# Kernel tuning notes

Hardware: AMD Instinct MI355X
Metric: run time of the kernel (lower is better)

Reference implementation:

```python
import jax, jax.numpy as jnp
import numpy as np

B, S, D, H, L, V = 2, 2048, 256, 4, 4, 50257
HD = D // H  # head_dim = 64


def layer_norm(x, scale, bias, eps=1e-5):
    m = jnp.mean(x, axis=-1, keepdims=True)
    v = jnp.var(x, axis=-1, keepdims=True)
    return (x - m) * jax.lax.rsqrt(v + eps) * scale + bias


def setup_inputs() -> dict:
    key = jax.random.key(0)
    ks = jax.random.split(key, 16)

    def w(k, shape, std=0.02):
        return (jax.random.normal(k, shape) * std).astype(jnp.float32)

    return {
        "input_ids": jax.random.randint(ks[0], (B, S), 0, V, dtype=jnp.int32),
        "tok_emb": w(ks[1], (V, D)),      # tied with lm_head
        "pos_emb": w(ks[2], (S, D)),
        # per-layer params stacked on leading L axis (scanned)
        "Wq": w(ks[3], (L, D, D)), "bq": jnp.zeros((L, D), jnp.float32),
        "Wk": w(ks[4], (L, D, D)), "bk": jnp.zeros((L, D), jnp.float32),
        "Wv": w(ks[5], (L, D, D)), "bv": jnp.zeros((L, D), jnp.float32),
        "Wo": w(ks[6], (L, D, D)), "bo": jnp.zeros((L, D), jnp.float32),
        "ln1_s": jnp.ones((L, D), jnp.float32), "ln1_b": jnp.zeros((L, D), jnp.float32),
        "ln2_s": jnp.ones((L, D), jnp.float32), "ln2_b": jnp.zeros((L, D), jnp.float32),
        "W1": w(ks[7], (L, D, 4 * D)), "b1": jnp.zeros((L, 4 * D), jnp.float32),
        "W2": w(ks[8], (L, 4 * D, D)), "b2": jnp.zeros((L, D), jnp.float32),
        "lnf_s": jnp.ones((D,), jnp.float32), "lnf_b": jnp.zeros((D,), jnp.float32),
    }


def _forward(input_ids, tok_emb, pos_emb, Wq, bq, Wk, bk, Wv, bv, Wo, bo,
             ln1_s, ln1_b, ln2_s, ln2_b, W1, b1, W2, b2, lnf_s, lnf_b):
    Bv, Sv = input_ids.shape
    h = tok_emb[input_ids] + pos_emb[:Sv][None, :, :]  # (B,S,D); dropout = eval no-op
    scale = HD ** -0.5
    causal = jnp.tril(jnp.ones((Sv, Sv), dtype=bool))  # (S,S)

    def block(h, p):
        wq, bq_, wk, bk_, wv, bv_, wo, bo_, s1, sb1, s2, sb2, wf1, bf1, wf2, bf2 = p
        n = layer_norm(h, s1, sb1)
        q = (n @ wq + bq_).reshape(Bv, Sv, H, HD)
        k = (n @ wk + bk_).reshape(Bv, Sv, H, HD)
        v = (n @ wv + bv_).reshape(Bv, Sv, H, HD)
        scores = jnp.einsum('bqhd,bkhd->bhqk', q, k) * scale  # (B,H,S,S)
        scores = jnp.where(causal, scores, -jnp.inf)
        attn = jax.nn.softmax(scores, axis=-1)  # attn dropout = eval no-op
        o = jnp.einsum('bhqk,bkhd->bqhd', attn, v).reshape(Bv, Sv, D)
        h = h + (o @ wo + bo_)
        n2 = layer_norm(h, s2, sb2)
        f = jax.nn.gelu(n2 @ wf1 + bf1, approximate=False) @ wf2 + bf2  # torch GELU = exact erf
        return h + f, None

    params = (Wq, bq, Wk, bk, Wv, bv, Wo, bo, ln1_s, ln1_b, ln2_s, ln2_b, W1, b1, W2, b2)
    h, _ = jax.lax.scan(block, h, params)
    h = layer_norm(h, lnf_s, lnf_b)
    return h @ tok_emb.T  # tied lm_head, (B,S,V)


def reference(input_ids, tok_emb, pos_emb, Wq, bq, Wk, bk, Wv, bv, Wo, bo,
              ln1_s, ln1_b, ln2_s, ln2_b, W1, b1, W2, b2, lnf_s, lnf_b):
    return _forward(input_ids, tok_emb, pos_emb, Wq, bq, Wk, bk, Wv, bv, Wo, bo,
                    ln1_s, ln1_b, ln2_s, ln2_b, W1, b1, W2, b2, lnf_s, lnf_b)
```

## Files before the change

kernel.cpp:

```cpp
#include <hip/hip_runtime.h>

#define BB   2
#define SS   2048
#define DD   256
#define HH   4
#define LL   4
#define VV   50257
#define HDIM 64
#define DFF  1024
#define BS   (BB*SS)

typedef unsigned short u16;
typedef unsigned int   u32;
typedef __attribute__((ext_vector_type(8))) short bf16x8;
typedef __attribute__((ext_vector_type(4))) float f32x4;

#define DEV static __device__ __forceinline__

DEV u16 f2bf(float f) {
    u32 x = __builtin_bit_cast(u32, f);
    x += 0x7fffu + ((x >> 16) & 1u);
    return (u16)(x >> 16);
}

DEV f32x4 zero4() { f32x4 v; v[0]=0.f; v[1]=0.f; v[2]=0.f; v[3]=0.f; return v; }

__global__ __launch_bounds__(256) void cvt_kernel(const float* __restrict__ in,
                                                  u16* __restrict__ out, int n4) {
    int i = blockIdx.x * 256 + threadIdx.x;
    if (i >= n4) return;
    float4 v = ((const float4*)in)[i];
    ushort4 o; o.x = f2bf(v.x); o.y = f2bf(v.y); o.z = f2bf(v.z); o.w = f2bf(v.w);
    ((ushort4*)out)[i] = o;
}

__global__ __launch_bounds__(256) void wtrans_kernel(const float* __restrict__ in,
                                                     u16* __restrict__ out, int K, int N) {
    __shared__ float tile[32][33];
    const size_t off = (size_t)blockIdx.z * K * N;
    in  += off; out += off;
    int tx = threadIdx.x, ty = threadIdx.y;
    int n0 = blockIdx.x * 32, k0 = blockIdx.y * 32;
    #pragma unroll
    for (int i = 0; i < 4; i++)
        tile[ty + 8*i][tx] = in[(size_t)(k0 + ty + 8*i) * N + n0 + tx];
    __syncthreads();
    #pragma unroll
    for (int i = 0; i < 4; i++)
        out[(size_t)(n0 + ty + 8*i) * K + k0 + tx] = f2bf(tile[tx][ty + 8*i]);
}

__global__ __launch_bounds__(256) void embed_kernel(const int* __restrict__ ids,
                                                    const float* __restrict__ te,
                                                    const float* __restrict__ pe,
                                                    float* __restrict__ h) {
    int i  = blockIdx.x * 256 + threadIdx.x;
    int bs = i >> 6, c = i & 63;
    int id = ids[bs];
    int sr = bs & (SS - 1);
    float4 t = ((const float4*)(te + (size_t)id * DD))[c];
    float4 p = ((const float4*)(pe + (size_t)sr * DD))[c];
    float4 r; r.x = t.x + p.x; r.y = t.y + p.y; r.z = t.z + p.z; r.w = t.w + p.w;
    ((float4*)h)[i] = r;
}

__global__ __launch_bounds__(256) void ln_kernel(const float* __restrict__ x,
                                                 const float* __restrict__ g,
                                                 const float* __restrict__ b,
                                                 u16* __restrict__ out) {
    const int wid = threadIdx.x >> 6, lane = threadIdx.x & 63;
    const int row = blockIdx.x * 4 + wid;
    const float4 v = ((const float4*)(x + (size_t)row * DD))[lane];
    float s = v.x + v.y + v.z + v.w;
    float q = v.x*v.x + v.y*v.y + v.z*v.z + v.w*v.w;
    #pragma unroll
    for (int m = 1; m < 64; m <<= 1) { s += __shfl_xor(s, m); q += __shfl_xor(q, m); }
    const float mean = s * (1.f / DD);
    const float var  = q * (1.f / DD) - mean * mean;
    const float rs   = rsqrtf(var + 1e-5f);
    const float4 gg = ((const float4*)g)[lane];
    const float4 bb = ((const float4*)b)[lane];
    ushort4 o;
    o.x = f2bf((v.x - mean) * rs * gg.x + bb.x);
    o.y = f2bf((v.y - mean) * rs * gg.y + bb.y);
    o.z = f2bf((v.z - mean) * rs * gg.z + bb.z);
    o.w = f2bf((v.w - mean) * rs * gg.w + bb.w);
    ((ushort4*)(out + (size_t)row * DD))[lane] = o;
}

template<int BM, int BN, int EPI>
__global__ __launch_bounds__(256) void gemm_kernel(const u16* __restrict__ A,
                                                   const u16* __restrict__ Bt,
                                                   const float* __restrict__ bias,
                                                   const float* res, void* outp,
                                                   int M, int N, int K) {
    constexpr int NI = BM / 32, NJ = BN / 32;
    __shared__ __align__(16) u16 As[BM * 72];
    __shared__ __align__(16) u16 Bs[BN * 72];
    const int tid = threadIdx.x;
    const int wid = tid >> 6, lane = tid & 63, quad = lane >> 4, l16 = lane & 15;
    const int m0 = blockIdx.y * BM, n0 = blockIdx.x * BN;
    const int wm = (wid >> 1) * (BM / 2), wn = (wid & 1) * (BN / 2);

    f32x4 acc[NI][NJ];
    #pragma unroll
    for (int i = 0; i < NI; i++)
        #pragma unroll
        for (int j = 0; j < NJ; j++) acc[i][j] = zero4();

    for (int k0 = 0; k0 < K; k0 += 64) {
        #pragma unroll
        for (int p = 0; p < BM / 32; p++) {
            int idx = p * 256 + tid, row = idx >> 3, c = (idx & 7) * 8;
            *(uint4*)(&As[row * 72 + c]) =
                *(const uint4*)(A + (size_t)(m0 + row) * K + k0 + c);
        }
        #pragma unroll
        for (int p = 0; p < BN / 32; p++) {
            int idx = p * 256 + tid, row = idx >> 3, c = (idx & 7) * 8;
            uint4 val{0, 0, 0, 0};
            if (EPI != 3 || (n0 + row) < N)
                val = *(const uint4*)(Bt + (size_t)(n0 + row) * K + k0 + c);
            *(uint4*)(&Bs[row * 72 + c]) = val;
        }
        __syncthreads();
        #pragma unroll
        for (int ks = 0; ks < 2; ks++) {
            bf16x8 af[NI], bfr[NJ];
            #pragma unroll
            for (int i = 0; i < NI; i++)
                af[i] = *(const bf16x8*)(&As[(wm + i*16 + l16) * 72 + ks*32 + quad*8]);
            #pragma unroll
            for (int j = 0; j < NJ; j++)
                bfr[j] = *(const bf16x8*)(&Bs[(wn + j*16 + l16) * 72 + ks*32 + quad*8]);
            #pragma unroll
            for (int i = 0; i < NI; i++)
                #pragma unroll
                for (int j = 0; j < NJ; j++)
                    acc[i][j] = __builtin_amdgcn_mfma_f32_16x16x32_bf16(
                        af[i], bfr[j], acc[i][j], 0, 0, 0);
        }
        __syncthreads();
    }

    #pragma unroll
    for (int i = 0; i < NI; i++) {
        #pragma unroll
        for (int j = 0; j < NJ; j++) {
            #pragma unroll
            for (int r = 0; r < 4; r++) {
                int row = m0 + wm + i*16 + quad*4 + r;
                int col = n0 + wn + j*16 + l16;
                float v = acc[i][j][r];
                if (EPI == 0) {
                    v += bias[col];
                    ((u16*)outp)[(size_t)row * N + col] = f2bf(v);
                } else if (EPI == 1) {
                    v += bias[col];
                    float gel = 0.5f * v * (1.f + erff(v * 0.70710678118654752f));
                    ((u16*)outp)[(size_t)row * N + col] = f2bf(gel);
                } else if (EPI == 2) {
                    v += bias[col] + res[(size_t)row * N + col];
                    ((float*)outp)[(size_t)row * N + col] = v;
                } else {
                    if (col < N) ((float*)outp)[(size_t)row * N + col] = v;
                }
            }
        }
    }
}

__global__ __launch_bounds__(256) void vtrans_kernel(const u16* __restrict__ v,
                                                     u16* __restrict__ vt) {
    __shared__ u16 tile[32][33];
    int bh = blockIdx.z, b = bh >> 2, hh = bh & 3;
    int s0 = blockIdx.x * 32, d0 = blockIdx.y * 32;
    int tx = threadIdx.x, ty = threadIdx.y;
    #pragma unroll
    for (int i = 0; i < 4; i++)
        tile[ty + 8*i][tx] = v[(size_t)(b*SS + s0 + ty + 8*i) * DD + hh*HDIM + d0 + tx];
    __syncthreads();
    #pragma unroll
    for (int i = 0; i < 4; i++)
        vt[(size_t)(bh*HDIM + d0 + ty + 8*i) * SS + s0 + tx] = tile[tx][ty + 8*i];
}

__global__ __launch_bounds__(256) void attn_kernel(const u16* __restrict__ q,
                                                   const u16* __restrict__ k,
                                                   const u16* __restrict__ vt,
                                                   u16* __restrict__ o) {
    const int tid = threadIdx.x;
    const int wid = tid >> 6, lane = tid & 63, quad = lane >> 4, l16 = lane & 15;
    const int bh = blockIdx.y, b = bh >> 2, hh = bh & 3;
    const int wgq0 = blockIdx.x * 64;
    const int wq0  = wgq0 + wid * 16;

    __shared__ __align__(16) u16 plds[4][16 * 40];

    const u16* qb = q  + (size_t)b * SS * DD + hh * HDIM;
    const u16* kb = k  + (size_t)b * SS * DD + hh * HDIM;
    const u16* vb = vt + (size_t)bh * HDIM * SS;

    bf16x8 qf0 = *(const bf16x8*)(qb + (size_t)(wq0 + l16) * DD + quad * 8);
    bf16x8 qf1 = *(const bf16x8*)(qb + (size_t)(wq0 + l16) * DD + 32 + quad * 8);

    f32x4 oacc[4];
    #pragma unroll
    for (int i = 0; i < 4; i++) oacc[i] = zero4();
    float mst[4], lst[4];
    #pragma unroll
    for (int r = 0; r < 4; r++) { mst[r] = -1e30f; lst[r] = 0.f; }

    const int nt = wgq0 / 32 + 2;
    for (int kt = 0; kt < nt; ++kt) {
        const int kv0 = kt * 32;
        f32x4 sc[2]; sc[0] = zero4(); sc[1] = zero4();
        #pragma unroll
        for (int t = 0; t < 2; t++) {
            const u16* kr = kb + (size_t)(kv0 + t*16 + l16) * DD + quad * 8;
            bf16x8 kf0 = *(const bf16x8*)(kr);
            bf16x8 kf1 = *(const bf16x8*)(kr + 32);
            sc[t] = __builtin_amdgcn_mfma_f32_16x16x32_bf16(qf0, kf0, sc[t], 0, 0, 0);
            sc[t] = __builtin_amdgcn_mfma_f32_16x16x32_bf16(qf1, kf1, sc[t], 0, 0, 0);
        }
        float mx[4];
        #pragma unroll
        for (int r = 0; r < 4; r++) {
            int qrow = wq0 + quad * 4 + r;
            float s0 = sc[0][r] * 0.125f; if (kv0 + l16 > qrow)      s0 = -1e30f;
            float s1 = sc[1][r] * 0.125f; if (kv0 + 16 + l16 > qrow) s1 = -1e30f;
            sc[0][r] = s0; sc[1][r] = s1;
            mx[r] = fmaxf(s0, s1);
        }
        #pragma unroll
        for (int m = 1; m < 16; m <<= 1) {
            #pragma unroll
            for (int r = 0; r < 4; r++) mx[r] = fmaxf(mx[r], __shfl_xor(mx[r], m));
        }
        float al[4], rsum[4];
        #pragma unroll
        for (int r = 0; r < 4; r++) {
            float mn = fmaxf(mst[r], mx[r]);
            al[r] = __expf(mst[r] - mn);
            mst[r] = mn;
            float p0 = __expf(sc[0][r] - mn);
            float p1 = __expf(sc[1][r] - mn);
            sc[0][r] = p0; sc[1][r] = p1;
            rsum[r] = p0 + p1;
        }
        #pragma unroll
        for (int m = 1; m < 16; m <<= 1) {
            #pragma unroll
            for (int r = 0; r < 4; r++) rsum[r] += __shfl_xor(rsum[r], m);
        }
        #pragma unroll
        for (int r = 0; r < 4; r++) lst[r] = lst[r] * al[r] + rsum[r];
        #pragma unroll
        for (int d4 = 0; d4 < 4; d4++)
            #pragma unroll
            for (int r = 0; r < 4; r++) oacc[d4][r] *= al[r];

        u16* pw = &plds[wid][0];
        #pragma unroll
        for (int r = 0; r < 4; r++) {
            pw[(quad*4 + r) * 40 + l16]      = f2bf(sc[0][r]);
            pw[(quad*4 + r) * 40 + 16 + l16] = f2bf(sc[1][r]);
        }
        __syncthreads();
        bf16x8 pf = *(const bf16x8*)(pw + l16 * 40 + quad * 8);
        #pragma unroll
        for (int d4 = 0; d4 < 4; d4++) {
            bf16x8 vf = *(const bf16x8*)(vb + (size_t)(d4*16 + l16) * SS + kv0 + quad * 8);
            oacc[d4] = __builtin_amdgcn_mfma_f32_16x16x32_bf16(pf, vf, oacc[d4], 0, 0, 0);
        }
        __syncthreads();
    }

    u16* ob = o + (size_t)b * SS * DD + hh * HDIM;
    #pragma unroll
    for (int d4 = 0; d4 < 4; d4++)
        #pragma unroll
        for (int r = 0; r < 4; r++) {
            float ov = oacc[d4][r] / lst[r];
            ob[(size_t)(wq0 + quad*4 + r) * DD + d4*16 + l16] = f2bf(ov);
        }
}

extern "C" void kernel_launch(void* const* d_in, const int* in_sizes, int n_in,
                              void* d_out, int out_size, void* d_ws, size_t ws_size,
                              hipStream_t stream) {
    (void)in_sizes; (void)n_in; (void)out_size; (void)ws_size;
    const int*   ids  = (const int*)  d_in[0];
    const float* temb = (const float*)d_in[1];
    const float* pemb = (const float*)d_in[2];
    const float* Wq = (const float*)d_in[3];  const float* bq = (const float*)d_in[4];
    const float* Wk = (const float*)d_in[5];  const float* bk = (const float*)d_in[6];
    const float* Wv = (const float*)d_in[7];  const float* bv = (const float*)d_in[8];
    const float* Wo = (const float*)d_in[9];  const float* bo = (const float*)d_in[10];
    const float* ln1s = (const float*)d_in[11]; const float* ln1b = (const float*)d_in[12];
    const float* ln2s = (const float*)d_in[13]; const float* ln2b = (const float*)d_in[14];
    const float* W1 = (const float*)d_in[15]; const float* b1 = (const float*)d_in[16];
    const float* W2 = (const float*)d_in[17]; const float* b2 = (const float*)d_in[18];
    const float* lnfs = (const float*)d_in[19]; const float* lnfb = (const float*)d_in[20];
    float* out = (float*)d_out;

    char* ws = (char*)d_ws;
    auto alloc = [&](size_t bytes) -> char* {
        char* p = ws; ws += (bytes + 255) & ~(size_t)255; return p;
    };
    u16* tembb = (u16*)alloc((size_t)VV * DD * 2);
    u16* wqt   = (u16*)alloc((size_t)LL * DD * DD * 2);
    u16* wkt   = (u16*)alloc((size_t)LL * DD * DD * 2);
    u16* wvt   = (u16*)alloc((size_t)LL * DD * DD * 2);
    u16* wot   = (u16*)alloc((size_t)LL * DD * DD * 2);
    u16* w1t   = (u16*)alloc((size_t)LL * DD * DFF * 2);
    u16* w2t   = (u16*)alloc((size_t)LL * DD * DFF * 2);
    float* h   = (float*)alloc((size_t)BS * DD * 4);
    u16* nbuf  = (u16*)alloc((size_t)BS * DD * 2);
    u16* qbuf  = (u16*)alloc((size_t)BS * DD * 2);
    u16* kbuf  = (u16*)alloc((size_t)BS * DD * 2);
    u16* vbuf  = (u16*)alloc((size_t)BS * DD * 2);
    u16* vtb   = (u16*)alloc((size_t)BS * DD * 2);
    u16* obuf  = (u16*)alloc((size_t)BS * DD * 2);
    u16* f1    = (u16*)alloc((size_t)BS * DFF * 2);

    cvt_kernel<<<(VV*DD/4 + 255)/256, 256, 0, stream>>>(temb, tembb, VV*DD/4);
    wtrans_kernel<<<dim3(DD/32, DD/32, LL),  dim3(32,8), 0, stream>>>(Wq, wqt, DD, DD);
    wtrans_kernel<<<dim3(DD/32, DD/32, LL),  dim3(32,8), 0, stream>>>(Wk, wkt, DD, DD);
    wtrans_kernel<<<dim3(DD/32, DD/32, LL),  dim3(32,8), 0, stream>>>(Wv, wvt, DD, DD);
    wtrans_kernel<<<dim3(DD/32, DD/32, LL),  dim3(32,8), 0, stream>>>(Wo, wot, DD, DD);
    wtrans_kernel<<<dim3(DFF/32, DD/32, LL), dim3(32,8), 0, stream>>>(W1, w1t, DD, DFF);
    wtrans_kernel<<<dim3(DD/32, DFF/32, LL), dim3(32,8), 0, stream>>>(W2, w2t, DFF, DD);

    embed_kernel<<<BS*DD/4/256, 256, 0, stream>>>(ids, temb, pemb, h);

    const dim3 gQ(DD/64, BS/64);
    for (int l = 0; l < LL; l++) {
        ln_kernel<<<BS/4, 256, 0, stream>>>(h, ln1s + l*DD, ln1b + l*DD, nbuf);
        gemm_kernel<64,64,0><<<gQ, 256, 0, stream>>>(nbuf, wqt + (size_t)l*DD*DD,
            bq + l*DD, nullptr, qbuf, BS, DD, DD);
        gemm_kernel<64,64,0><<<gQ, 256, 0, stream>>>(nbuf, wkt + (size_t)l*DD*DD,
            bk + l*DD, nullptr, kbuf, BS, DD, DD);
        gemm_kernel<64,64,0><<<gQ, 256, 0, stream>>>(nbuf, wvt + (size_t)l*DD*DD,
            bv + l*DD, nullptr, vbuf, BS, DD, DD);
        vtrans_kernel<<<dim3(SS/32, HDIM/32, BB*HH), dim3(32,8), 0, stream>>>(vbuf, vtb);
        attn_kernel<<<dim3(SS/64, BB*HH), 256, 0, stream>>>(qbuf, kbuf, vtb, obuf);
        gemm_kernel<64,64,2><<<gQ, 256, 0, stream>>>(obuf, wot + (size_t)l*DD*DD,
            bo + l*DD, h, h, BS, DD, DD);
        ln_kernel<<<BS/4, 256, 0, stream>>>(h, ln2s + l*DD, ln2b + l*DD, nbuf);
        gemm_kernel<128,128,1><<<dim3(DFF/128, BS/128), 256, 0, stream>>>(nbuf,
            w1t + (size_t)l*DD*DFF, b1 + l*DFF, nullptr, f1, BS, DFF, DD);
        gemm_kernel<64,64,2><<<gQ, 256, 0, stream>>>(f1, w2t + (size_t)l*DD*DFF,
            b2 + l*DD, h, h, BS, DD, DFF);
    }
    ln_kernel<<<BS/4, 256, 0, stream>>>(h, lnfs, lnfb, nbuf);
    gemm_kernel<128,128,3><<<dim3((VV + 127)/128, BS/128), 256, 0, stream>>>(nbuf,
        tembb, nullptr, nullptr, out, BS, VV, DD);
}
```

Before: 1.859 ms.

## Fuse QKV projections into one GEMM and streamline attention inner loop

Concatenates Wq/Wk/Wv (and biases) into a single 768-wide weight so one GEMM produces Q, K and V into an interleaved buffer, removing two launches and re-reads of the normalized input. The attention kernel reads Q/K directly from this buffer with stride 768, prefetches the next K tile, loads V before the score MFMAs, and drops block-wide barriers since each wave uses its own LDS region. Each wave now iterates only over key tiles up to its own causal limit, skipping fully masked work. Relies on intra-wave LDS write/read ordering without a barrier.

```diff
diff --git a/kernel.cpp b/kernel.cpp
--- a/kernel.cpp
+++ b/kernel.cpp
@@ -9,6 +9,7 @@
 #define HDIM 64
 #define DFF  1024
 #define BS   (BB*SS)
+#define QKVS 768
 
 typedef unsigned short u16;
 typedef unsigned int   u32;
@@ -35,10 +36,11 @@
 }
 
 __global__ __launch_bounds__(256) void wtrans_kernel(const float* __restrict__ in,
-                                                     u16* __restrict__ out, int K, int N) {
+                                                     u16* __restrict__ out, int K, int N,
+                                                     size_t outLS) {
     __shared__ float tile[32][33];
-    const size_t off = (size_t)blockIdx.z * K * N;
-    in  += off; out += off;
+    in  += (size_t)blockIdx.z * K * N;
+    out += (size_t)blockIdx.z * outLS;
     int tx = threadIdx.x, ty = threadIdx.y;
     int n0 = blockIdx.x * 32, k0 = blockIdx.y * 32;
     #pragma unroll
@@ -48,6 +50,20 @@
     #pragma unroll
     for (int i = 0; i < 4; i++)
         out[(size_t)(n0 + ty + 8*i) * K + k0 + tx] = f2bf(tile[tx][ty + 8*i]);
+}
+
+__global__ __launch_bounds__(256) void bias_concat(const float* __restrict__ bq,
+                                                   const float* __restrict__ bk,
+                                                   const float* __restrict__ bv,
+                                                   float* __restrict__ out) {
+    int i = blockIdx.x * 256 + threadIdx.x;
+    if (i >= LL * QKVS) return;
+    int l = i / QKVS, c = i - l * QKVS;
+    float v;
+    if (c < DD)           v = bq[l * DD + c];
+    else if (c < 2 * DD)  v = bk[l * DD + c - DD];
+    else                  v = bv[l * DD + c - 2 * DD];
+    out[i] = v;
 }
 
 __global__ __launch_bounds__(256) void embed_kernel(const int* __restrict__ ids,
@@ -170,7 +186,7 @@
     }
 }
 
-__global__ __launch_bounds__(256) void vtrans_kernel(const u16* __restrict__ v,
+__global__ __launch_bounds__(256) void vtrans_kernel(const u16* __restrict__ qkv,
                                                      u16* __restrict__ vt) {
     __shared__ u16 tile[32][33];
     int bh = blockIdx.z, b = bh >> 2, hh = bh & 3;
@@ -178,58 +194,73 @@
     int tx = threadIdx.x, ty = threadIdx.y;
     #pragma unroll
     for (int i = 0; i < 4; i++)
-        tile[ty + 8*i][tx] = v[(size_t)(b*SS + s0 + ty + 8*i) * DD + hh*HDIM + d0 + tx];
+        tile[ty + 8*i][tx] =
+            qkv[(size_t)(b*SS + s0 + ty + 8*i) * QKVS + 2*DD + hh*HDIM + d0 + tx];
     __syncthreads();
     #pragma unroll
     for (int i = 0; i < 4; i++)
         vt[(size_t)(bh*HDIM + d0 + ty + 8*i) * SS + s0 + tx] = tile[tx][ty + 8*i];
 }
 
-__global__ __launch_bounds__(256) void attn_kernel(const u16* __restrict__ q,
-                                                   const u16* __restrict__ k,
+__global__ __launch_bounds__(256) void attn_kernel(const u16* __restrict__ qkv,
                                                    const u16* __restrict__ vt,
                                                    u16* __restrict__ o) {
     const int tid = threadIdx.x;
     const int wid = tid >> 6, lane = tid & 63, quad = lane >> 4, l16 = lane & 15;
     const int bh = blockIdx.y, b = bh >> 2, hh = bh & 3;
-    const int wgq0 = blockIdx.x * 64;
-    const int wq0  = wgq0 + wid * 16;
+    const int wq0 = blockIdx.x * 64 + wid * 16;
 
     __shared__ __align__(16) u16 plds[4][16 * 40];
 
-    const u16* qb = q  + (size_t)b * SS * DD + hh * HDIM;
-    const u16* kb = k  + (size_t)b * SS * DD + hh * HDIM;
+    const u16* qb = qkv + (size_t)b * SS * QKVS + hh * HDIM;
+    const u16* kb = qb + DD;
     const u16* vb = vt + (size_t)bh * HDIM * SS;
 
-    bf16x8 qf0 = *(const bf16x8*)(qb + (size_t)(wq0 + l16) * DD + quad * 8);
-    bf16x8 qf1 = *(const bf16x8*)(qb + (size_t)(wq0 + l16) * DD + 32 + quad * 8);
-
-    f32x4 oacc[4];
-    #pragma unroll
-    for (int i = 0; i < 4; i++) oacc[i] = zero4();
+    bf16x8 qf0 = *(const bf16x8*)(qb + (size_t)(wq0 + l16) * QKVS + quad * 8);
+    bf16x8 qf1 = *(const bf16x8*)(qb + (size_t)(wq0 + l16) * QKVS + 32 + quad * 8);
+
+    f32x4 oacc0 = zero4(), oacc1 = zero4(), oacc2 = zero4(), oacc3 = zero4();
     float mst[4], lst[4];
     #pragma unroll
     for (int r = 0; r < 4; r++) { mst[r] = -1e30f; lst[r] = 0.f; }
 
-    const int nt = wgq0 / 32 + 2;
+    const int nt = (wq0 >> 5) + 1;
+
+    const u16* krow = kb + (size_t)l16 * QKVS + quad * 8;
+    bf16x8 kc0 = *(const bf16x8*)(krow);
+    bf16x8 kc1 = *(const bf16x8*)(krow + 32);
+    bf16x8 kc2 = *(const bf16x8*)(krow + (size_t)16 * QKVS);
+    bf16x8 kc3 = *(const bf16x8*)(krow + (size_t)16 * QKVS + 32);
+
     for (int kt = 0; kt < nt; ++kt) {
         const int kv0 = kt * 32;
-        f32x4 sc[2]; sc[0] = zero4(); sc[1] = zero4();
-        #pragma unroll
-        for (int t = 0; t < 2; t++) {
-            const u16* kr = kb + (size_t)(kv0 + t*16 + l16) * DD + quad * 8;
-            bf16x8 kf0 = *(const bf16x8*)(kr);
-            bf16x8 kf1 = *(const bf16x8*)(kr + 32);
-            sc[t] = __builtin_amdgcn_mfma_f32_16x16x32_bf16(qf0, kf0, sc[t], 0, 0, 0);
-            sc[t] = __builtin_amdgcn_mfma_f32_16x16x32_bf16(qf1, kf1, sc[t], 0, 0, 0);
-        }
-        float mx[4];
+
+        bf16x8 vf0 = *(const bf16x8*)(vb + (size_t)(     l16) * SS + kv0 + quad * 8);
+        bf16x8 vf1 = *(const bf16x8*)(vb + (size_t)(16 + l16) * SS + kv0 + quad * 8);
+        bf16x8 vf2 = *(const bf16x8*)(vb + (size_t)(32 + l16) * SS + kv0 + quad * 8);
+        bf16x8 vf3 = *(const bf16x8*)(vb + (size_t)(48 + l16) * SS + kv0 + quad * 8);
+
+        f32x4 sc0 = zero4(), sc1 = zero4();
+        sc0 = __builtin_amdgcn_mfma_f32_16x16x32_bf16(qf0, kc0, sc0, 0, 0, 0);
+        sc0 = __builtin_amdgcn_mfma_f32_16x16x32_bf16(qf1, kc1, sc0, 0, 0, 0);
+        sc1 = __builtin_amdgcn_mfma_f32_16x16x32_bf16(qf0, kc2, sc1, 0, 0, 0);
+        sc1 = __builtin_amdgcn_mfma_f32_16x16x32_bf16(qf1, kc3, sc1, 0, 0, 0);
+
+        if (kt + 1 < nt) {
+            const u16* kr = kb + (size_t)(kv0 + 32 + l16) * QKVS + quad * 8;
+            kc0 = *(const bf16x8*)(kr);
+            kc1 = *(const bf16x8*)(kr + 32);
+            kc2 = *(const bf16x8*)(kr + (size_t)16 * QKVS);
+            kc3 = *(const bf16x8*)(kr + (size_t)16 * QKVS + 32);
+        }
+
+        float p0[4], p1[4], mx[4];
         #pragma unroll
         for (int r = 0; r < 4; r++) {
             int qrow = wq0 + quad * 4 + r;
-            float s0 = sc[0][r] * 0.125f; if (kv0 + l16 > qrow)      s0 = -1e30f;
-            float s1 = sc[1][r] * 0.125f; if (kv0 + 16 + l16 > qrow) s1 = -1e30f;
-            sc[0][r] = s0; sc[1][r] = s1;
+            float s0 = sc0[r] * 0.125f; if (kv0 + l16 > qrow)      s0 = -1e30f;
+            float s1 = sc1[r] * 0.125f; if (kv0 + 16 + l16 > qrow) s1 = -1e30f;
+            p0[r] = s0; p1[r] = s1;
             mx[r] = fmaxf(s0, s1);
         }
         #pragma unroll
@@ -243,10 +274,10 @@
             float mn = fmaxf(mst[r], mx[r]);
             al[r] = __expf(mst[r] - mn);
             mst[r] = mn;
-            float p0 = __expf(sc[0][r] - mn);
-            float p1 = __expf(sc[1][r] - mn);
-            sc[0][r] = p0; sc[1][r] = p1;
-            rsum[r] = p0 + p1;
+            float e0 = __expf(p0[r] - mn);
+            float e1 = __expf(p1[r] - mn);
+            p0[r] = e0; p1[r] = e1;
+            rsum[r] = e0 + e1;
         }
         #pragma unroll
         for (int m = 1; m < 16; m <<= 1) {
@@ -254,36 +285,35 @@
             for (int r = 0; r < 4; r++) rsum[r] += __shfl_xor(rsum[r], m);
         }
         #pragma unroll
-        for (int r = 0; r < 4; r++) lst[r] = lst[r] * al[r] + rsum[r];
-        #pragma unroll
-        for (int d4 = 0; d4 < 4; d4++)
-            #pragma unroll
-            for (int r = 0; r < 4; r++) oacc[d4][r] *= al[r];
+        for (int r = 0; r < 4; r++) {
+            lst[r] = lst[r] * al[r] + rsum[r];
+            oacc0[r] *= al[r]; oacc1[r] *= al[r];
+            oacc2[r] *= al[r]; oacc3[r] *= al[r];
+        }
 
         u16* pw = &plds[wid][0];
         #pragma unroll
         for (int r = 0; r < 4; r++) {
-            pw[(quad*4 + r) * 40 + l16]      = f2bf(sc[0][r]);
-            pw[(quad*4 + r) * 40 + 16 + l16] = f2bf(sc[1][r]);
-        }
-        __syncthreads();
+            pw[(quad*4 + r) * 40 + l16]      = f2bf(p0[r]);
+            pw[(quad*4 + r) * 40 + 16 + l16] = f2bf(p1[r]);
+        }
         bf16x8 pf = *(const bf16x8*)(pw + l16 * 40 + quad * 8);
-        #pragma unroll
-        for (int d4 = 0; d4 < 4; d4++) {
-            bf16x8 vf = *(const bf16x8*)(vb + (size_t)(d4*16 + l16) * SS + kv0 + quad * 8);
-            oacc[d4] = __builtin_amdgcn_mfma_f32_16x16x32_bf16(pf, vf, oacc[d4], 0, 0, 0);
-        }
-        __syncthreads();
+        oacc0 = __builtin_amdgcn_mfma_f32_16x16x32_bf16(pf, vf0, oacc0, 0, 0, 0);
+        oacc1 = __builtin_amdgcn_mfma_f32_16x16x32_bf16(pf, vf1, oacc1, 0, 0, 0);
+        oacc2 = __builtin_amdgcn_mfma_f32_16x16x32_bf16(pf, vf2, oacc2, 0, 0, 0);
+        oacc3 = __builtin_amdgcn_mfma_f32_16x16x32_bf16(pf, vf3, oacc3, 0, 0, 0);
     }
 
     u16* ob = o + (size_t)b * SS * DD + hh * HDIM;
     #pragma unroll
-    for (int d4 = 0; d4 < 4; d4++)
-        #pragma unroll
-        for (int r = 0; r < 4; r++) {
-            float ov = oacc[d4][r] / lst[r];
-            ob[(size_t)(wq0 + quad*4 + r) * DD + d4*16 + l16] = f2bf(ov);
-        }
+    for (int r = 0; r < 4; r++) {
+        const float inv = 1.f / lst[r];
+        const size_t row = (size_t)(wq0 + quad*4 + r) * DD;
+        ob[row +  0 + l16] = f2bf(oacc0[r] * inv);
+        ob[row + 16 + l16] = f2bf(oacc1[r] * inv);
+        ob[row + 32 + l16] = f2bf(oacc2[r] * inv);
+        ob[row + 48 + l16] = f2bf(oacc3[r] * inv);
+    }
 }
 
 extern "C" void kernel_launch(void* const* d_in, const int* in_sizes, int n_in,
@@ -309,42 +339,44 @@
         char* p = ws; ws += (bytes + 255) & ~(size_t)255; return p;
     };
     u16* tembb = (u16*)alloc((size_t)VV * DD * 2);
-    u16* wqt   = (u16*)alloc((size_t)LL * DD * DD * 2);
-    u16* wkt   = (u16*)alloc((size_t)LL * DD * DD * 2);
-    u16* wvt   = (u16*)alloc((size_t)LL * DD * DD * 2);
+    u16* wqkvt = (u16*)alloc((size_t)LL * QKVS * DD * 2);
     u16* wot   = (u16*)alloc((size_t)LL * DD * DD * 2);
     u16* w1t   = (u16*)alloc((size_t)LL * DD * DFF * 2);
     u16* w2t   = (u16*)alloc((size_t)LL * DD * DFF * 2);
+    float* bqkv= (float*)alloc((size_t)LL * QKVS * 4);
     float* h   = (float*)alloc((size_t)BS * DD * 4);
     u16* nbuf  = (u16*)alloc((size_t)BS * DD * 2);
-    u16* qbuf  = (u16*)alloc((size_t)BS * DD * 2);
-    u16* kbuf  = (u16*)alloc((size_t)BS * DD * 2);
-    u16* vbuf  = (u16*)alloc((size_t)BS * DD * 2);
+    u16* qkv   = (u16*)alloc((size_t)BS * QKVS * 2);
     u16* vtb   = (u16*)alloc((size_t)BS * DD * 2);
     u16* obuf  = (u16*)alloc((size_t)BS * DD * 2);
     u16* f1    = (u16*)alloc((size_t)BS * DFF * 2);
 
     cvt_kernel<<<(VV*DD/4 + 255)/256, 256, 0, stream>>>(temb, tembb, VV*DD/4);
-    wtrans_kernel<<<dim3(DD/32, DD/32, LL),  dim3(32,8), 0, stream>>>(Wq, wqt, DD, DD);
-    wtrans_kernel<<<dim3(DD/32, DD/32, LL),  dim3(32,8), 0, stream>>>(Wk, wkt, DD, DD);
-    wtrans_kernel<<<dim3(DD/32, DD/32, LL),  dim3(32,8), 0, stream>>>(Wv, wvt, DD, DD);
-    wtrans_kernel<<<dim3(DD/32, DD/32, LL),  dim3(32,8), 0, stream>>>(Wo, wot, DD, DD);
-    wtrans_kernel<<<dim3(DFF/32, DD/32, LL), dim3(32,8), 0, stream>>>(W1, w1t, DD, DFF);
-    wtrans_kernel<<<dim3(DD/32, DFF/32, LL), dim3(32,8), 0, stream>>>(W2, w2t, DFF, DD);
+    const dim3 wtB(32, 8);
+    wtrans_kernel<<<dim3(DD/32, DD/32, LL), wtB, 0, stream>>>(
+        Wq, wqkvt,             DD, DD, (size_t)QKVS * DD);
+    wtrans_kernel<<<dim3(DD/32, DD/32, LL), wtB, 0, stream>>>(
+        Wk, wqkvt + DD*DD,     DD, DD, (size_t)QKVS * DD);
+    wtrans_kernel<<<dim3(DD/32, DD/32, LL), wtB, 0, stream>>>(
+        Wv, wqkvt + 2*DD*DD,   DD, DD, (size_t)QKVS * DD);
+    wtrans_kernel<<<dim3(DD/32, DD/32, LL), wtB, 0, stream>>>(
+        Wo, wot, DD, DD, (size_t)DD * DD);
+    wtrans_kernel<<<dim3(DFF/32, DD/32, LL), wtB, 0, stream>>>(
+        W1, w1t, DD, DFF, (size_t)DD * DFF);
+    wtrans_kernel<<<dim3(DD/32, DFF/32, LL), wtB, 0, stream>>>(
+        W2, w2t, DFF, DD, (size_t)DD * DFF);
+    bias_concat<<<(LL*QKVS + 255)/256, 256, 0, stream>>>(bq, bk, bv, bqkv);
 
     embed_kernel<<<BS*DD/4/256, 256, 0, stream>>>(ids, temb, pemb, h);
 
     const dim3 gQ(DD/64, BS/64);
     for (int l = 0; l < LL; l++) {
         ln_kernel<<<BS/4, 256, 0, stream>>>(h, ln1s + l*DD, ln1b + l*DD, nbuf);
-        gemm_kernel<64,64,0><<<gQ, 256, 0, stream>>>(nbuf, wqt + (size_t)l*DD*DD,
-            bq + l*DD, nullptr, qbuf, BS, DD, DD);
-        gemm_kernel<64,64,0><<<gQ, 256, 0, stream>>>(nbuf, wkt + (size_t)l*DD*DD,
-            bk + l*DD, nullptr, kbuf, BS, DD, DD);
-        gemm_kernel<64,64,0><<<gQ, 256, 0, stream>>>(nbuf, wvt + (size_t)l*DD*DD,
-            bv + l*DD, nullptr, vbuf, BS, DD, DD);
-        vtrans_kernel<<<dim3(SS/32, HDIM/32, BB*HH), dim3(32,8), 0, stream>>>(vbuf, vtb);
-        attn_kernel<<<dim3(SS/64, BB*HH), 256, 0, stream>>>(qbuf, kbuf, vtb, obuf);
+        gemm_kernel<64,64,0><<<dim3(QKVS/64, BS/64), 256, 0, stream>>>(nbuf,
+            wqkvt + (size_t)l*QKVS*DD, bqkv + (size_t)l*QKVS, nullptr, qkv,
+            BS, QKVS, DD);
+        vtrans_kernel<<<dim3(SS/32, HDIM/32, BB*HH), wtB, 0, stream>>>(qkv, vtb);
+        attn_kernel<<<dim3(SS/64, BB*HH), 256, 0, stream>>>(qkv, vtb, obuf);
         gemm_kernel<64,64,2><<<gQ, 256, 0, stream>>>(obuf, wot + (size_t)l*DD*DD,
             bo + l*DD, h, h, BS, DD, DD);
         ln_kernel<<<BS/4, 256, 0, stream>>>(h, ln2s + l*DD, ln2b + l*DD, nbuf);
```

Result: faster. 1.619 ms (-12.9%).
